# Kernel tuning notes

Hardware: AMD Instinct MI355X
Metric: run time of the kernel (lower is better)

The kernel has to match this reference:

```python
import jax, jax.numpy as jnp
import numpy as np

NNODES = 16384
DIM = 512
ALPHA = 3.0
K = 10  # min(scale_hyperedges=10, nnodes)


def setup_inputs() -> dict:
    key = jax.random.key(0)
    k1, k2, k3 = jax.random.split(key, 3)
    return {
        "idx": jnp.arange(NNODES, dtype=jnp.int32),
        # nn.Embedding default init: N(0, 1)
        "emb_weight": jax.random.normal(k1, (NNODES, DIM), dtype=jnp.float32),
        # nn.Linear default init scale ~ 1/sqrt(fan_in)
        "lin_w": jax.random.uniform(k2, (DIM, DIM), dtype=jnp.float32,
                                    minval=-1.0, maxval=1.0) / np.float32(np.sqrt(DIM)),
        "lin_b": jax.random.uniform(k3, (DIM,), dtype=jnp.float32,
                                    minval=-1.0, maxval=1.0) / np.float32(np.sqrt(DIM)),
    }


def reference(idx, emb_weight, lin_w, lin_b):
    # node_features = emb1(idx)                      [N, D]
    feats = emb_weight[idx]
    # transformed = tanh(alpha * lin1(feats))        [N, D]
    t = jnp.tanh(ALPHA * (feats @ lin_w.T + lin_b))
    # sim = T @ T^T                                  [N, N]
    sim = t @ t.T
    # top-k most similar nodes per row
    _, top_idx = jax.lax.top_k(sim, K)               # [N, K]
    n = emb_weight.shape[0]
    rows = jnp.arange(n)[:, None]                    # [N, 1]
    # H[i, top_idx[i]] = 1, then transpose -> incidence [nodes, hyperedges]
    H = jnp.zeros((n, n), dtype=t.dtype).at[rows, top_idx].set(1.0)
    return H.T
```

## Files before the change

kernel.cpp:

```cpp
#include <hip/hip_runtime.h>
#include <hip/hip_bf16.h>
#include <math.h>

#define NN 16384
#define DD 512
#define KSEL 10
#define MCAND 16
#define NSPLIT 4
#define RESCORE 16

typedef __bf16 bf16x8 __attribute__((ext_vector_type(8)));
typedef float  f32x4  __attribute__((ext_vector_type(4)));

#define GLOAD_LDS16(gsrc, ldst) \
    __builtin_amdgcn_global_load_lds( \
        (const __attribute__((address_space(1))) void*)(gsrc), \
        (__attribute__((address_space(3))) void*)(ldst), 16, 0, 0)

__global__ __launch_bounds__(256) void k_transform(
    const int* __restrict__ idx, const float* __restrict__ emb,
    const float* __restrict__ W, const float* __restrict__ bias,
    float* __restrict__ t_out, unsigned short* __restrict__ tb_out)
{
    __shared__ float As[32][68];
    __shared__ float Bs[32][68];
    const int tid = threadIdx.x;
    const int tx = tid & 15, ty = tid >> 4;
    const int m0 = (blockIdx.x >> 3) << 6;
    const int n0 = (blockIdx.x & 7) << 6;

    float acc[4][4] = {};

    const int f0 = tid, f1 = tid + 256;
    const int r0 = f0 >> 3, c0_ = f0 & 7;
    const int r1 = f1 >> 3, c1_ = f1 & 7;
    const int ga0 = idx[m0 + r0];
    const int ga1 = idx[m0 + r1];

    for (int kc = 0; kc < DD; kc += 32) {
        const float4 a0 = *(const float4*)&emb[(size_t)ga0 * DD + kc + (c0_ << 2)];
        const float4 a1 = *(const float4*)&emb[(size_t)ga1 * DD + kc + (c1_ << 2)];
        const float4 b0 = *(const float4*)&W[(size_t)(n0 + r0) * DD + kc + (c0_ << 2)];
        const float4 b1 = *(const float4*)&W[(size_t)(n0 + r1) * DD + kc + (c1_ << 2)];
        As[(c0_<<2)+0][r0] = a0.x; As[(c0_<<2)+1][r0] = a0.y;
        As[(c0_<<2)+2][r0] = a0.z; As[(c0_<<2)+3][r0] = a0.w;
        As[(c1_<<2)+0][r1] = a1.x; As[(c1_<<2)+1][r1] = a1.y;
        As[(c1_<<2)+2][r1] = a1.z; As[(c1_<<2)+3][r1] = a1.w;
        Bs[(c0_<<2)+0][r0] = b0.x; Bs[(c0_<<2)+1][r0] = b0.y;
        Bs[(c0_<<2)+2][r0] = b0.z; Bs[(c0_<<2)+3][r0] = b0.w;
        Bs[(c1_<<2)+0][r1] = b1.x; Bs[(c1_<<2)+1][r1] = b1.y;
        Bs[(c1_<<2)+2][r1] = b1.z; Bs[(c1_<<2)+3][r1] = b1.w;
        __syncthreads();
        #pragma unroll
        for (int k = 0; k < 32; ++k) {
            const float4 a = *(const float4*)&As[k][ty << 2];
            const float4 b = *(const float4*)&Bs[k][tx << 2];
            const float av[4] = {a.x, a.y, a.z, a.w};
            const float bv[4] = {b.x, b.y, b.z, b.w};
            #pragma unroll
            for (int i = 0; i < 4; ++i)
                #pragma unroll
                for (int j = 0; j < 4; ++j)
                    acc[i][j] = fmaf(av[i], bv[j], acc[i][j]);
        }
        __syncthreads();
    }

    #pragma unroll
    for (int i = 0; i < 4; ++i) {
        const int m = m0 + (ty << 2) + i;
        float o[4];
        union { __hip_bfloat16 h[4]; ushort4 u; } cc;
        #pragma unroll
        for (int j = 0; j < 4; ++j) {
            const int n = n0 + (tx << 2) + j;
            o[j] = tanhf(3.0f * (acc[i][j] + bias[n]));
            cc.h[j] = __float2bfloat16(o[j]);
        }
        *(float4*)&t_out[(size_t)m * DD + n0 + (tx << 2)] =
            make_float4(o[0], o[1], o[2], o[3]);
        *(ushort4*)&tb_out[(size_t)m * DD + n0 + (tx << 2)] = cc.u;
    }
}

__global__ __launch_bounds__(512) void k_sim_topk(
    const unsigned short* __restrict__ tb,
    float* __restrict__ pv, unsigned short* __restrict__ pi)
{
    __shared__ __align__(16) char SM[124928];
    float*          topv   = (float*)(SM + 98304);
    unsigned short* topi   = (unsigned short*)(SM + 114688);
    float*          thresh = (float*)(SM + 122880);
    int*            cnt    = (int*)(SM + 123904);
    float*          cv     = (float*)(SM);
    int*            ci     = (int*)(SM + 36864);

    const int tid  = threadIdx.x;
    const int wave = tid >> 6;
    const int lane = tid & 63;
    const int wr   = wave >> 1;
    const int wc   = wave & 1;

    const int bid  = blockIdx.x;
    const int s    = (bid & 7) >> 1;
    const int mblk = ((bid & 1) << 5) | (bid >> 3);
    const int m0   = mblk << 8;
    const int c_begin = s * (NN / NSPLIT);

    if (tid < 256) {
        thresh[tid] = -1e30f;
        cnt[tid] = 0;
        #pragma unroll
        for (int j = 0; j < MCAND; ++j) { topv[tid*MCAND + j] = -1e30f; topi[tid*MCAND + j] = 0xFFFFu; }
    }
    __syncthreads();

    const char* tbb = (const char*)tb;
    const int l4r = lane >> 2;
    const int l4u = lane & 3;

    for (int ct = 0; ct < (NN / NSPLIT) / 128; ++ct) {
        const int c0 = c_begin + (ct << 7);
        f32x4 acc[4][4] = {};

        auto STAGE = [&](int k) {
            const int rb = k & 3;
            const size_t kb = (size_t)k << 6;
            char* Ad = SM + (rb << 14);
            char* Bd = SM + 65536 + (rb << 13);
            #pragma unroll
            for (int i_ = 0; i_ < 2; ++i_) {
                const int rl = (wave << 5) + (i_ << 4) + l4r;
                GLOAD_LDS16(tbb + (size_t)(m0 + rl) * 1024 + kb + ((size_t)(l4u ^ ((rl >> 1) & 3)) << 4),
                            Ad + (wave << 11) + (i_ << 10));
            }
            {
                const int rl = (wave << 4) + l4r;
                GLOAD_LDS16(tbb + (size_t)(c0 + rl) * 1024 + kb + ((size_t)(l4u ^ ((rl >> 1) & 3)) << 4),
                            Bd + (wave << 10));
            }
        };

        auto COMPUTE = [&](int k) {
            const int rb = k & 3;
            const char* Ac = SM + (rb << 14);
            const char* Bc = SM + 65536 + (rb << 13);
            const int u = lane >> 4;
            bf16x8 af[4], bf[4];
            #pragma unroll
            for (int m = 0; m < 4; ++m) {
                const int row = (wr << 6) + (m << 4) + (lane & 15);
                af[m] = *(const bf16x8*)(Ac + (row << 6) + ((u ^ ((row >> 1) & 3)) << 4));
            }
            #pragma unroll
            for (int n = 0; n < 4; ++n) {
                const int row = (wc << 6) + (n << 4) + (lane & 15);
                bf[n] = *(const bf16x8*)(Bc + (row << 6) + ((u ^ ((row >> 1) & 3)) << 4));
            }
            #pragma unroll
            for (int m = 0; m < 4; ++m)
                #pragma unroll
                for (int n = 0; n < 4; ++n)
                    acc[m][n] = __builtin_amdgcn_mfma_f32_16x16x32_bf16(
                        af[m], bf[n], acc[m][n], 0, 0, 0);
        };

        STAGE(0); STAGE(1);
        for (int kc = 0; kc < 14; ++kc) {
            asm volatile("s_waitcnt vmcnt(3)" ::: "memory");
            __builtin_amdgcn_s_barrier();
            STAGE(kc + 2);
            COMPUTE(kc);
        }
        asm volatile("s_waitcnt vmcnt(3)" ::: "memory");
        __builtin_amdgcn_s_barrier();
        COMPUTE(14);
        asm volatile("s_waitcnt vmcnt(0)" ::: "memory");
        __builtin_amdgcn_s_barrier();
        COMPUTE(15);

        __syncthreads();

        #pragma unroll
        for (int rnd = 0; rnd < 4; ++rnd) {
            const int wcr = rnd >> 1;
            const int nf0 = (rnd & 1) << 1;
            if (wc == wcr) {
                #pragma unroll
                for (int m = 0; m < 4; ++m) {
                    #pragma unroll
                    for (int nn = 0; nn < 2; ++nn) {
                        #pragma unroll
                        for (int j = 0; j < 4; ++j) {
                            const int row = (wr << 6) + (m << 4) + ((lane >> 4) << 2) + j;
                            const float v = acc[m][nf0 + nn][j];
                            if (v >= thresh[row]) {
                                const int p = atomicAdd(&cnt[row], 1);
                                cv[row * 33 + p] = v;
                                ci[row * 33 + p] = c0 + (wcr << 6) + ((nf0 + nn) << 4) + (lane & 15);
                            }
                        }
                    }
                }
            }
            __syncthreads();
            if (tid < 256) {
                const int r = tid;
                const int n_ = cnt[r];
                float* tv = &topv[r * MCAND];
                unsigned short* ti = &topi[r * MCAND];
                for (int q = 0; q < n_; ++q) {
                    const float v = cv[r * 33 + q];
                    const unsigned short c = (unsigned short)ci[r * 33 + q];
                    if (v > tv[MCAND-1] || (v == tv[MCAND-1] && c < ti[MCAND-1])) {
                        int p = MCAND - 1;
                        while (p > 0 && (v > tv[p-1] || (v == tv[p-1] && c < ti[p-1]))) {
                            tv[p] = tv[p-1]; ti[p] = ti[p-1]; --p;
                        }
                        tv[p] = v; ti[p] = c;
                    }
                }
                cnt[r] = 0;
                thresh[r] = tv[MCAND-1];
            }
            __syncthreads();
        }
    }

    if (tid < 256) {
        const size_t base = (((size_t)s * 64 + mblk) * 256 + tid) * MCAND;
        #pragma unroll
        for (int j = 0; j < MCAND; ++j) {
            pv[base + j] = topv[tid * MCAND + j];
            pi[base + j] = topi[tid * MCAND + j];
        }
    }
}

__global__ __launch_bounds__(256) void k_rescore(
    const float* __restrict__ t, const float* __restrict__ pv,
    const unsigned short* __restrict__ pi, float* __restrict__ out)
{
    const int wave = threadIdx.x >> 6;
    const int lane = threadIdx.x & 63;
    const int r = blockIdx.x * 4 + wave;
    const int mblk = r >> 8, local = r & 255;

    const int sp = lane >> 4, slot = lane & 15;
    const size_t cbase = (((size_t)sp * 64 + mblk) * 256 + local) * MCAND;
    const float v = pv[cbase + slot];
    const unsigned int idxc = pi[cbase + slot];
    const unsigned int u = __float_as_uint(v);
    const unsigned int mkey = (u & 0x80000000u) ? ~u : (u | 0x80000000u);
    unsigned long long key = ((unsigned long long)mkey << 16) |
                             (unsigned long long)((~idxc) & 0xFFFFu);

    #pragma unroll
    for (int k = 2; k <= 64; k <<= 1) {
        #pragma unroll
        for (int j = k >> 1; j > 0; j >>= 1) {
            const unsigned long long other = __shfl_xor(key, j, 64);
            const bool lower = (lane & j) == 0;
            const bool ascBlock = (lane & k) == 0;
            const bool takeMax = (lower == ascBlock);
            const bool mineBigger = key > other;
            key = (takeMax == mineBigger) ? key : other;
        }
    }
    const int cid = (int)((~(unsigned int)key) & 0xFFFFu);

    const float4 a0 = *(const float4*)&t[(size_t)r * DD + lane * 8];
    const float4 a1 = *(const float4*)&t[(size_t)r * DD + lane * 8 + 4];

    double bestv[KSEL];
    int    besti[KSEL];
    #pragma unroll
    for (int j = 0; j < KSEL; ++j) { bestv[j] = -1e300; besti[j] = 0x7fffffff; }

    for (int q = 0; q < RESCORE; ++q) {
        const int c = __shfl(cid, q, 64);
        const float4 v0 = *(const float4*)&t[(size_t)c * DD + lane * 8];
        const float4 v1 = *(const float4*)&t[(size_t)c * DD + lane * 8 + 4];
        double sdot = 0.0;
        sdot += (double)a0.x * (double)v0.x;
        sdot += (double)a0.y * (double)v0.y;
        sdot += (double)a0.z * (double)v0.z;
        sdot += (double)a0.w * (double)v0.w;
        sdot += (double)a1.x * (double)v1.x;
        sdot += (double)a1.y * (double)v1.y;
        sdot += (double)a1.z * (double)v1.z;
        sdot += (double)a1.w * (double)v1.w;
        #pragma unroll
        for (int off = 32; off > 0; off >>= 1)
            sdot += __shfl_down(sdot, off, 64);
        if (lane == 0) {
            if (sdot > bestv[KSEL-1] || (sdot == bestv[KSEL-1] && c < besti[KSEL-1])) {
                int p = KSEL - 1;
                while (p > 0 && (sdot > bestv[p-1] ||
                                 (sdot == bestv[p-1] && c < besti[p-1]))) {
                    bestv[p] = bestv[p-1]; besti[p] = besti[p-1]; --p;
                }
                bestv[p] = sdot; besti[p] = c;
            }
        }
    }

    if (lane == 0) {
        #pragma unroll
        for (int j = 0; j < KSEL; ++j)
            out[(size_t)besti[j] * NN + r] = 1.0f;
    }
}

extern "C" void kernel_launch(void* const* d_in, const int* in_sizes, int n_in,
                              void* d_out, int out_size, void* d_ws, size_t ws_size,
                              hipStream_t stream) {
    const int*   idx  = (const int*)d_in[0];
    const float* emb  = (const float*)d_in[1];
    const float* linw = (const float*)d_in[2];
    const float* linb = (const float*)d_in[3];
    float* out = (float*)d_out;

    float*          t  = (float*)d_ws;
    unsigned short* tb = (unsigned short*)((char*)d_ws + (size_t)32 * 1024 * 1024);
    float*          pv = (float*)((char*)d_ws + (size_t)48 * 1024 * 1024);
    unsigned short* pi = (unsigned short*)((char*)d_ws + (size_t)52 * 1024 * 1024);

    (void)hipMemsetAsync(d_out, 0, (size_t)NN * (size_t)NN * sizeof(float), stream);

    k_transform<<<dim3(256 * 8), dim3(256), 0, stream>>>(idx, emb, linw, linb, t, tb);
    k_sim_topk<<<dim3(256), dim3(512), 0, stream>>>(tb, pv, pi);
    k_rescore<<<dim3(NN / 4), dim3(256), 0, stream>>>(t, pv, pi, out);
}
```

Baseline: 2.321 ms.

## Shrink sim-topk tiles to 128-row panels with more splits and triple buffering

The similarity/top-k kernel now processes 128-row panels with 256 threads instead of 256-row panels with 512 threads, and splits the columns 8 ways instead of 4. The grid grows from 256 to 1024 blocks. LDS staging drops from a 4-deep to a 3-deep ring, and per-split candidates fall from 16 to 8, so LDS use shrinks from about 122 KB to 55 KB. The aim is more resident blocks per CU and better latency hiding for the candidate-selection phase. The cost is less A-tile reuse per block, and a small risk of missing true top-10 neighbours if more than 8 of them fall in one 2048-column split.

```diff
diff --git a/kernel.cpp b/kernel.cpp
--- a/kernel.cpp
+++ b/kernel.cpp
@@ -5,8 +5,9 @@
 #define NN 16384
 #define DD 512
 #define KSEL 10
-#define MCAND 16
-#define NSPLIT 4
+#define MCAND 8
+#define NSPLIT 8
+#define NPANEL 128
 #define RESCORE 16
 
 typedef __bf16 bf16x8 __attribute__((ext_vector_type(8)));
@@ -83,17 +84,17 @@
     }
 }
 
-__global__ __launch_bounds__(512) void k_sim_topk(
+__global__ __launch_bounds__(256) void k_sim_topk(
     const unsigned short* __restrict__ tb,
     float* __restrict__ pv, unsigned short* __restrict__ pi)
 {
-    __shared__ __align__(16) char SM[124928];
-    float*          topv   = (float*)(SM + 98304);
-    unsigned short* topi   = (unsigned short*)(SM + 114688);
-    float*          thresh = (float*)(SM + 122880);
-    int*            cnt    = (int*)(SM + 123904);
+    __shared__ __align__(16) char SM[56320];
+    float*          topv   = (float*)(SM + 49152);
+    unsigned short* topi   = (unsigned short*)(SM + 53248);
+    float*          thresh = (float*)(SM + 55296);
+    int*            cnt    = (int*)(SM + 55808);
     float*          cv     = (float*)(SM);
-    int*            ci     = (int*)(SM + 36864);
+    int*            ci     = (int*)(SM + 16896);
 
     const int tid  = threadIdx.x;
     const int wave = tid >> 6;
@@ -102,12 +103,12 @@
     const int wc   = wave & 1;
 
     const int bid  = blockIdx.x;
-    const int s    = (bid & 7) >> 1;
-    const int mblk = ((bid & 1) << 5) | (bid >> 3);
-    const int m0   = mblk << 8;
+    const int s    = bid & 7;
+    const int mblk = bid >> 3;
+    const int m0   = mblk << 7;
     const int c_begin = s * (NN / NSPLIT);
 
-    if (tid < 256) {
+    if (tid < 128) {
         thresh[tid] = -1e30f;
         cnt[tid] = 0;
         #pragma unroll
@@ -124,27 +125,25 @@
         f32x4 acc[4][4] = {};
 
         auto STAGE = [&](int k) {
-            const int rb = k & 3;
+            const int rb = k % 3;
             const size_t kb = (size_t)k << 6;
-            char* Ad = SM + (rb << 14);
-            char* Bd = SM + 65536 + (rb << 13);
+            char* Ad = SM + rb * 16384;
+            char* Bd = Ad + 8192;
             #pragma unroll
             for (int i_ = 0; i_ < 2; ++i_) {
-                const int rl = (wave << 5) + (i_ << 4) + l4r;
+                const int ai = (wave << 1) + i_;
+                const int rl = (ai << 4) + l4r;
                 GLOAD_LDS16(tbb + (size_t)(m0 + rl) * 1024 + kb + ((size_t)(l4u ^ ((rl >> 1) & 3)) << 4),
-                            Ad + (wave << 11) + (i_ << 10));
-            }
-            {
-                const int rl = (wave << 4) + l4r;
+                            Ad + (ai << 10));
                 GLOAD_LDS16(tbb + (size_t)(c0 + rl) * 1024 + kb + ((size_t)(l4u ^ ((rl >> 1) & 3)) << 4),
-                            Bd + (wave << 10));
+                            Bd + (ai << 10));
             }
         };
 
         auto COMPUTE = [&](int k) {
-            const int rb = k & 3;
-            const char* Ac = SM + (rb << 14);
-            const char* Bc = SM + 65536 + (rb << 13);
+            const int rb = k % 3;
+            const char* Ac = SM + rb * 16384;
+            const char* Bc = Ac + 8192;
             const int u = lane >> 4;
             bf16x8 af[4], bf[4];
             #pragma unroll
@@ -167,12 +166,12 @@
 
         STAGE(0); STAGE(1);
         for (int kc = 0; kc < 14; ++kc) {
-            asm volatile("s_waitcnt vmcnt(3)" ::: "memory");
+            asm volatile("s_waitcnt vmcnt(4)" ::: "memory");
             __builtin_amdgcn_s_barrier();
             STAGE(kc + 2);
             COMPUTE(kc);
         }
-        asm volatile("s_waitcnt vmcnt(3)" ::: "memory");
+        asm volatile("s_waitcnt vmcnt(4)" ::: "memory");
         __builtin_amdgcn_s_barrier();
         COMPUTE(14);
         asm volatile("s_waitcnt vmcnt(0)" ::: "memory");
@@ -204,7 +203,7 @@
                 }
             }
             __syncthreads();
-            if (tid < 256) {
+            if (tid < 128) {
                 const int r = tid;
                 const int n_ = cnt[r];
                 float* tv = &topv[r * MCAND];
@@ -227,8 +226,8 @@
         }
     }
 
-    if (tid < 256) {
-        const size_t base = (((size_t)s * 64 + mblk) * 256 + tid) * MCAND;
+    if (tid < 128) {
+        const size_t base = (((size_t)s * NPANEL + mblk) * 128 + tid) * MCAND;
         #pragma unroll
         for (int j = 0; j < MCAND; ++j) {
             pv[base + j] = topv[tid * MCAND + j];
@@ -244,10 +243,10 @@
     const int wave = threadIdx.x >> 6;
     const int lane = threadIdx.x & 63;
     const int r = blockIdx.x * 4 + wave;
-    const int mblk = r >> 8, local = r & 255;
-
-    const int sp = lane >> 4, slot = lane & 15;
-    const size_t cbase = (((size_t)sp * 64 + mblk) * 256 + local) * MCAND;
+    const int panel = r >> 7, local = r & 127;
+
+    const int sp = lane >> 3, slot = lane & 7;
+    const size_t cbase = (((size_t)sp * NPANEL + panel) * 128 + local) * MCAND;
     const float v = pv[cbase + slot];
     const unsigned int idxc = pi[cbase + slot];
     const unsigned int u = __float_as_uint(v);
@@ -329,6 +328,6 @@
     (void)hipMemsetAsync(d_out, 0, (size_t)NN * (size_t)NN * sizeof(float), stream);
 
     k_transform<<<dim3(256 * 8), dim3(256), 0, stream>>>(idx, emb, linw, linb, t, tb);
-    k_sim_topk<<<dim3(256), dim3(512), 0, stream>>>(tb, pv, pi);
+    k_sim_topk<<<dim3(NPANEL * NSPLIT), dim3(256), 0, stream>>>(tb, pv, pi);
     k_rescore<<<dim3(NN / 4), dim3(256), 0, stream>>>(t, pv, pi, out);
 }
```

Result: slower. 2.618 ms (+12.8%).
